# Optimization experiments

Hardware: AMD Instinct MI355X
Metric: run time of the kernel (lower is better)

Reference implementation:

```python
import jax, jax.numpy as jnp
import numpy as np

D_NODE, D_EDGE, D_HEAD = 256, 128, 32
LN_EPS = 1e-5


def setup_inputs() -> dict:
    key = jax.random.key(0)
    ks = jax.random.split(key, 10)
    B, N = 1, 512
    s_node = 1.0 / np.sqrt(D_NODE)
    s_hh = 1.0 / np.sqrt(D_HEAD * D_HEAD)
    return {
        "node": jax.random.normal(ks[0], (B, N, D_NODE), dtype=jnp.float32),
        "edge": jax.random.normal(ks[1], (B, N, N, D_EDGE), dtype=jnp.float32),
        "ln_w": jnp.ones((D_NODE,), dtype=jnp.float32),
        "ln_b": jnp.zeros((D_NODE,), dtype=jnp.float32),
        "w_left": jax.random.normal(ks[2], (D_NODE, D_HEAD), dtype=jnp.float32) * s_node,
        "b_left": jax.random.normal(ks[3], (D_HEAD,), dtype=jnp.float32) * 0.02,
        "w_right": jax.random.normal(ks[4], (D_NODE, D_HEAD), dtype=jnp.float32) * s_node,
        "b_right": jax.random.normal(ks[5], (D_HEAD,), dtype=jnp.float32) * 0.02,
        "w_out": jax.random.normal(ks[6], (D_HEAD * D_HEAD, D_EDGE), dtype=jnp.float32) * s_hh,
        "b_out": jax.random.normal(ks[7], (D_EDGE,), dtype=jnp.float32) * 0.02,
    }


def reference(node, edge, ln_w, ln_b, w_left, b_left, w_right, b_right, w_out, b_out):
    # LayerNorm over d_node
    mu = jnp.mean(node, axis=-1, keepdims=True)
    var = jnp.mean(jnp.square(node - mu), axis=-1, keepdims=True)
    x = (node - mu) * jax.lax.rsqrt(var + LN_EPS) * ln_w + ln_b

    left = x @ w_left + b_left    # [B, N, d_head]
    right = x @ w_right + b_right  # [B, N, d_head]

    # Outer product flattened over (i,j) then projected to d_edge.
    # Fused: reshape w_out to [i, j, e] and contract directly, avoiding the
    # explicit [B, N, N, d_head*d_head] intermediate (same math as
    # einsum('bni,bmj->bnmij').flatten(-2) @ w_out).
    w3 = w_out.reshape(D_HEAD, D_HEAD, D_EDGE)
    out = jnp.einsum("bni,bmj,ije->bnme", left, right, w3) + b_out
    return out + edge
```

## Files before the change

### kernel.cpp

```cpp
#include <hip/hip_runtime.h>

#define D_NODE 256
#define D_EDGE 128
#define D_HEAD 32
#define NN 512

__global__ __launch_bounds__(256) void ln_proj_kernel(
    const float* __restrict__ node, const float* __restrict__ ln_w,
    const float* __restrict__ ln_b, const float* __restrict__ w_left,
    const float* __restrict__ b_left, const float* __restrict__ w_right,
    const float* __restrict__ b_right, float* __restrict__ left,
    float* __restrict__ right) {
  __shared__ float xs[D_NODE];
  __shared__ float red[10];
  const int n = blockIdx.x;
  const int t = threadIdx.x;
  float v = node[n * D_NODE + t];
  float s = v, ss = v * v;
#pragma unroll
  for (int o = 32; o > 0; o >>= 1) {
    s += __shfl_down(s, o);
    ss += __shfl_down(ss, o);
  }
  if ((t & 63) == 0) {
    red[t >> 6] = s;
    red[4 + (t >> 6)] = ss;
  }
  __syncthreads();
  if (t == 0) {
    float S = red[0] + red[1] + red[2] + red[3];
    float SS = red[4] + red[5] + red[6] + red[7];
    float mu = S * (1.0f / D_NODE);
    float var = SS * (1.0f / D_NODE) - mu * mu;
    red[8] = mu;
    red[9] = rsqrtf(var + 1e-5f);
  }
  __syncthreads();
  const float mu = red[8], rs = red[9];
  xs[t] = (v - mu) * rs * ln_w[t] + ln_b[t];
  __syncthreads();
  if (t < 64) {
    const int c = t & 31;
    const bool isL = (t < 32);
    const float* w = isL ? w_left : w_right;
    float acc = isL ? b_left[c] : b_right[c];
#pragma unroll 8
    for (int d = 0; d < D_NODE; ++d) acc = fmaf(xs[d], w[d * D_HEAD + c], acc);
    (isL ? left : right)[n * D_HEAD + c] = acc;
  }
}

__global__ __launch_bounds__(128) void rw_kernel(
    const float* __restrict__ right, const float* __restrict__ w_out,
    float* __restrict__ tmp) {
  const int m0 = blockIdx.x * 2;
  const int ibase = blockIdx.y * 16;
  const int t = threadIdx.x;
  const int e4 = t & 31;
  const int io = t >> 5;
  const float* r0 = right + m0 * D_HEAD;
  const float* r1 = r0 + D_HEAD;
  for (int k = 0; k < 4; ++k) {
    const int i = ibase + io * 4 + k;
    const float4* wp = (const float4*)(w_out + i * D_HEAD * D_EDGE) + e4;
    float4 a0 = {0.f, 0.f, 0.f, 0.f};
    float4 a1 = {0.f, 0.f, 0.f, 0.f};
#pragma unroll
    for (int j = 0; j < D_HEAD; ++j) {
      const float4 w4 = wp[j * (D_EDGE / 4)];
      const float rj0 = r0[j];
      const float rj1 = r1[j];
      a0.x = fmaf(rj0, w4.x, a0.x);
      a0.y = fmaf(rj0, w4.y, a0.y);
      a0.z = fmaf(rj0, w4.z, a0.z);
      a0.w = fmaf(rj0, w4.w, a0.w);
      a1.x = fmaf(rj1, w4.x, a1.x);
      a1.y = fmaf(rj1, w4.y, a1.y);
      a1.z = fmaf(rj1, w4.z, a1.z);
      a1.w = fmaf(rj1, w4.w, a1.w);
    }
    ((float4*)(tmp + (m0 * D_HEAD + i) * D_EDGE))[e4] = a0;
    ((float4*)(tmp + ((m0 + 1) * D_HEAD + i) * D_EDGE))[e4] = a1;
  }
}

__global__ __launch_bounds__(128) void fuse_kernel(
    const float* __restrict__ left, const float* __restrict__ tmp,
    const float* __restrict__ b_out, const float* __restrict__ edge,
    float* __restrict__ out) {
  const int m = blockIdx.x;
  const int n0 = blockIdx.y * 128;
  const int t = threadIdx.x;
  const int e2 = t & 63;
  const int nsub = __builtin_amdgcn_readfirstlane(t >> 6);
  float2 rT[D_HEAD];
  const float2* tp = (const float2*)(tmp + m * D_HEAD * D_EDGE) + e2;
#pragma unroll
  for (int i = 0; i < D_HEAD; ++i) rT[i] = tp[i * (D_EDGE / 2)];
  const float2 be = ((const float2*)b_out)[e2];
  const float2* edge2 = (const float2*)edge;
  float2* out2 = (float2*)out;
  const int stride = 2 * NN * (D_EDGE / 2);
  int idx = ((n0 + nsub) * NN + m) * (D_EDGE / 2) + e2;
  float2 ev = edge2[idx];
  for (int nn = nsub; nn < 128; nn += 2) {
    const int nidx = idx + stride;
    const int pidx = (nn + 2 < 128) ? nidx : idx;
    const float2 evn = edge2[pidx];
    const float* lp = left + (n0 + nn) * D_HEAD;
    float2 acc = be;
#pragma unroll
    for (int i = 0; i < D_HEAD; ++i) {
      const float l = lp[i];
      acc.x = fmaf(l, rT[i].x, acc.x);
      acc.y = fmaf(l, rT[i].y, acc.y);
    }
    acc.x += ev.x;
    acc.y += ev.y;
    out2[idx] = acc;
    ev = evn;
    idx = nidx;
  }
}

extern "C" void kernel_launch(void* const* d_in, const int* in_sizes, int n_in,
                              void* d_out, int out_size, void* d_ws, size_t ws_size,
                              hipStream_t stream) {
  const float* node    = (const float*)d_in[0];
  const float* edge    = (const float*)d_in[1];
  const float* ln_w    = (const float*)d_in[2];
  const float* ln_b    = (const float*)d_in[3];
  const float* w_left  = (const float*)d_in[4];
  const float* b_left  = (const float*)d_in[5];
  const float* w_right = (const float*)d_in[6];
  const float* b_right = (const float*)d_in[7];
  const float* w_out   = (const float*)d_in[8];
  const float* b_out   = (const float*)d_in[9];
  float* out = (float*)d_out;

  float* left  = (float*)d_ws;
  float* right = left + NN * D_HEAD;
  float* tmp   = right + NN * D_HEAD;

  ln_proj_kernel<<<NN, 256, 0, stream>>>(node, ln_w, ln_b, w_left, b_left,
                                         w_right, b_right, left, right);
  rw_kernel<<<dim3(NN / 2, 2), 128, 0, stream>>>(right, w_out, tmp);
  fuse_kernel<<<dim3(NN, 4), 128, 0, stream>>>(left, tmp, b_out, edge, out);
}
```

Baseline: 288.2 us.

## Restructure fuse kernel to batch edge loads and transpose left projection

The projection reduction in ln_proj is now split across all 256 threads using shared-memory partial sums, and the left projection is stored transposed. rw_kernel now computes one m per block with 256 threads. fuse_kernel moves to 8192 blocks of 256 threads, where each wave issues all 8 edge row loads up front and accumulates 8 rows against the tmp rows it streams. The aim is more memory-level parallelism and occupancy for the bandwidth-bound edge read/write. The cost is that tmp is now reread by many more blocks.

```diff
diff --git a/kernel.cpp b/kernel.cpp
--- a/kernel.cpp
+++ b/kernel.cpp
@@ -9,10 +9,11 @@
     const float* __restrict__ node, const float* __restrict__ ln_w,
     const float* __restrict__ ln_b, const float* __restrict__ w_left,
     const float* __restrict__ b_left, const float* __restrict__ w_right,
-    const float* __restrict__ b_right, float* __restrict__ left,
+    const float* __restrict__ b_right, float* __restrict__ leftT,
     float* __restrict__ right) {
   __shared__ float xs[D_NODE];
   __shared__ float red[10];
+  __shared__ float part[4][64];
   const int n = blockIdx.x;
   const int t = threadIdx.x;
   float v = node[n * D_NODE + t];
@@ -39,87 +40,96 @@
   const float mu = red[8], rs = red[9];
   xs[t] = (v - mu) * rs * ln_w[t] + ln_b[t];
   __syncthreads();
+  {
+    const int col = t & 63;
+    const int q = t >> 6;
+    const int c = col & 31;
+    const float* w = (col < 32) ? w_left : w_right;
+    float acc = 0.f;
+    const int d0 = q * 64;
+#pragma unroll 8
+    for (int d = d0; d < d0 + 64; ++d) acc = fmaf(xs[d], w[d * D_HEAD + c], acc);
+    part[q][col] = acc;
+  }
+  __syncthreads();
   if (t < 64) {
     const int c = t & 31;
     const bool isL = (t < 32);
-    const float* w = isL ? w_left : w_right;
-    float acc = isL ? b_left[c] : b_right[c];
-#pragma unroll 8
-    for (int d = 0; d < D_NODE; ++d) acc = fmaf(xs[d], w[d * D_HEAD + c], acc);
-    (isL ? left : right)[n * D_HEAD + c] = acc;
+    float acc = part[0][t] + part[1][t] + part[2][t] + part[3][t] +
+                (isL ? b_left[c] : b_right[c]);
+    if (isL)
+      leftT[c * NN + n] = acc;
+    else
+      right[n * D_HEAD + c] = acc;
   }
 }
 
-__global__ __launch_bounds__(128) void rw_kernel(
+__global__ __launch_bounds__(256) void rw_kernel(
     const float* __restrict__ right, const float* __restrict__ w_out,
     float* __restrict__ tmp) {
-  const int m0 = blockIdx.x * 2;
-  const int ibase = blockIdx.y * 16;
+  const int m = blockIdx.x;
   const int t = threadIdx.x;
   const int e4 = t & 31;
-  const int io = t >> 5;
-  const float* r0 = right + m0 * D_HEAD;
-  const float* r1 = r0 + D_HEAD;
+  const int i8 = t >> 5;
+  const float* r = right + m * D_HEAD;
+#pragma unroll
   for (int k = 0; k < 4; ++k) {
-    const int i = ibase + io * 4 + k;
+    const int i = i8 * 4 + k;
     const float4* wp = (const float4*)(w_out + i * D_HEAD * D_EDGE) + e4;
-    float4 a0 = {0.f, 0.f, 0.f, 0.f};
-    float4 a1 = {0.f, 0.f, 0.f, 0.f};
+    float4 a = {0.f, 0.f, 0.f, 0.f};
 #pragma unroll
     for (int j = 0; j < D_HEAD; ++j) {
       const float4 w4 = wp[j * (D_EDGE / 4)];
-      const float rj0 = r0[j];
-      const float rj1 = r1[j];
-      a0.x = fmaf(rj0, w4.x, a0.x);
-      a0.y = fmaf(rj0, w4.y, a0.y);
-      a0.z = fmaf(rj0, w4.z, a0.z);
-      a0.w = fmaf(rj0, w4.w, a0.w);
-      a1.x = fmaf(rj1, w4.x, a1.x);
-      a1.y = fmaf(rj1, w4.y, a1.y);
-      a1.z = fmaf(rj1, w4.z, a1.z);
-      a1.w = fmaf(rj1, w4.w, a1.w);
+      const float rj = r[j];
+      a.x = fmaf(rj, w4.x, a.x);
+      a.y = fmaf(rj, w4.y, a.y);
+      a.z = fmaf(rj, w4.z, a.z);
+      a.w = fmaf(rj, w4.w, a.w);
     }
-    ((float4*)(tmp + (m0 * D_HEAD + i) * D_EDGE))[e4] = a0;
-    ((float4*)(tmp + ((m0 + 1) * D_HEAD + i) * D_EDGE))[e4] = a1;
+    ((float4*)(tmp + (m * D_HEAD + i) * D_EDGE))[e4] = a;
   }
 }
 
-__global__ __launch_bounds__(128) void fuse_kernel(
-    const float* __restrict__ left, const float* __restrict__ tmp,
+__global__ __launch_bounds__(256) void fuse_kernel(
+    const float* __restrict__ leftT, const float* __restrict__ tmp,
     const float* __restrict__ b_out, const float* __restrict__ edge,
     float* __restrict__ out) {
   const int m = blockIdx.x;
-  const int n0 = blockIdx.y * 128;
-  const int t = threadIdx.x;
-  const int e2 = t & 63;
-  const int nsub = __builtin_amdgcn_readfirstlane(t >> 6);
-  float2 rT[D_HEAD];
-  const float2* tp = (const float2*)(tmp + m * D_HEAD * D_EDGE) + e2;
-#pragma unroll
-  for (int i = 0; i < D_HEAD; ++i) rT[i] = tp[i * (D_EDGE / 2)];
-  const float2 be = ((const float2*)b_out)[e2];
+  const int wave = __builtin_amdgcn_readfirstlane(threadIdx.x >> 6);
+  const int lane = threadIdx.x & 63;
+  const int nbase = blockIdx.y * 32 + wave * 8;
+
+  const float2* tp = (const float2*)(tmp + m * D_HEAD * D_EDGE) + lane;
+  const float2 be = ((const float2*)b_out)[lane];
   const float2* edge2 = (const float2*)edge;
   float2* out2 = (float2*)out;
-  const int stride = 2 * NN * (D_EDGE / 2);
-  int idx = ((n0 + nsub) * NN + m) * (D_EDGE / 2) + e2;
-  float2 ev = edge2[idx];
-  for (int nn = nsub; nn < 128; nn += 2) {
-    const int nidx = idx + stride;
-    const int pidx = (nn + 2 < 128) ? nidx : idx;
-    const float2 evn = edge2[pidx];
-    const float* lp = left + (n0 + nn) * D_HEAD;
-    float2 acc = be;
+  const long rowstride = (long)NN * (D_EDGE / 2);
+  const long base = ((long)nbase * NN + m) * (D_EDGE / 2) + lane;
+
+  float2 ed[8];
 #pragma unroll
-    for (int i = 0; i < D_HEAD; ++i) {
-      const float l = lp[i];
-      acc.x = fmaf(l, rT[i].x, acc.x);
-      acc.y = fmaf(l, rT[i].y, acc.y);
+  for (int r = 0; r < 8; ++r) ed[r] = edge2[base + r * rowstride];
+
+  float2 acc[8];
+#pragma unroll
+  for (int r = 0; r < 8; ++r) acc[r] = be;
+
+  const float* lB = leftT + nbase;
+#pragma unroll
+  for (int i = 0; i < D_HEAD; ++i) {
+    const float2 rt = tp[i * (D_EDGE / 2)];
+#pragma unroll
+    for (int r = 0; r < 8; ++r) {
+      const float l = lB[i * NN + r];
+      acc[r].x = fmaf(l, rt.x, acc[r].x);
+      acc[r].y = fmaf(l, rt.y, acc[r].y);
     }
-    acc.x += ev.x;
-    acc.y += ev.y;
-    out2[idx] = acc;
-    ev = evn;
-    idx = nidx;
+  }
+#pragma unroll
+  for (int r = 0; r < 8; ++r) {
+    acc[r].x += ed[r].x;
+    acc[r].y += ed[r].y;
+    out2[base + r * rowstride] = acc[r];
   }
 }
 
@@ -138,12 +148,12 @@
   const float* b_out   = (const float*)d_in[9];
   float* out = (float*)d_out;
 
-  float* left  = (float*)d_ws;
-  float* right = left + NN * D_HEAD;
+  float* leftT = (float*)d_ws;
+  float* right = leftT + D_HEAD * NN;
   float* tmp   = right + NN * D_HEAD;
 
   ln_proj_kernel<<<NN, 256, 0, stream>>>(node, ln_w, ln_b, w_left, b_left,
-                                         w_right, b_right, left, right);
-  rw_kernel<<<dim3(NN / 2, 2), 128, 0, stream>>>(right, w_out, tmp);
-  fuse_kernel<<<dim3(NN, 4), 128, 0, stream>>>(left, tmp, b_out, edge, out);
+                                         w_right, b_right, leftT, right);
+  rw_kernel<<<NN, 256, 0, stream>>>(right, w_out, tmp);
+  fuse_kernel<<<dim3(NN, 16), 256, 0, stream>>>(leftT, tmp, b_out, edge, out);
 }
```

New measurement: 280.8 us. 2.6% less time.
